# Kernel optimization log

Hardware: AMD Instinct MI355X
Metric: run time of the kernel (lower is better)

Reference implementation:

```python
import jax, jax.numpy as jnp
import numpy as np

B, IN_DIM, UNITS, NUM_K, NUM_S = 4096, 128, 256, 64, 256


def setup_inputs() -> dict:
    key = jax.random.key(0)
    ks = jax.random.split(key, 24)
    d = {
        "X": jax.random.normal(ks[0], (B, IN_DIM), jnp.float32),
        "h_prev": jax.random.normal(ks[1], (B, UNITS), jnp.float32),
        "c_prev": jax.random.normal(ks[2], (B, UNITS), jnp.float32),
        "M_prev": jax.random.normal(ks[3], (B, NUM_K, NUM_S), jnp.float32),
        "k_prev": jax.random.normal(ks[4], (B, NUM_S), jnp.float32),
    }
    rows = IN_DIM + UNITS
    s = 0.05
    d["Wf"] = jax.random.normal(ks[5], (rows, UNITS), jnp.float32) * s
    d["Wt"] = jax.random.normal(ks[6], (rows, UNITS), jnp.float32) * s
    d["Wi"] = jax.random.normal(ks[7], (rows, UNITS), jnp.float32) * s
    d["Wo"] = jax.random.normal(ks[8], (rows, UNITS), jnp.float32) * s
    d["bf"] = jnp.zeros((UNITS,), jnp.float32)
    d["bt"] = jnp.zeros((UNITS,), jnp.float32)
    d["bi"] = jnp.zeros((UNITS,), jnp.float32)
    d["bo"] = jnp.zeros((UNITS,), jnp.float32)
    d["Wk"] = jax.random.normal(ks[9], (UNITS, NUM_S), jnp.float32) * s
    d["bk"] = jnp.zeros((NUM_S,), jnp.float32)
    d["Wr"] = jax.random.normal(ks[10], (NUM_S, UNITS), jnp.float32) * s
    d["Wc"] = jax.random.normal(ks[11], (UNITS, UNITS), jnp.float32) * s
    d["Wh"] = jax.random.normal(ks[12], (NUM_S, UNITS), jnp.float32) * s
    d["We"] = jax.random.normal(ks[13], (UNITS, NUM_S), jnp.float32) * s
    d["be"] = jnp.zeros((NUM_S,), jnp.float32)
    d["Wa"] = jax.random.normal(ks[14], (UNITS, NUM_S), jnp.float32) * s
    d["ba"] = jnp.zeros((NUM_S,), jnp.float32)
    return d


def _l2n(x):
    # matches tf.nn.l2_normalize: x / sqrt(max(sum(x^2), eps))
    return x / jnp.sqrt(jnp.maximum(jnp.sum(x * x, axis=-1, keepdims=True), 1e-12))


def reference(X, h_prev, c_prev, M_prev, k_prev,
              Wf, Wt, Wi, Wo, bf, bt, bi, bo,
              Wk, bk, Wr, Wc, Wh, We, be, Wa, ba):
    sig = jax.nn.sigmoid
    xh = jnp.concatenate([X, h_prev], axis=-1)          # (B, in+units)
    i = sig(xh @ Wi + bi)
    f = sig(xh @ Wf + bf)
    o = sig(xh @ Wo + bo)
    t = sig(xh @ Wt + bt)
    c = f * c_prev + i * t                              # (B, units)

    # tf.keras.losses.cosine_similarity returns NEGATIVE cosine similarity
    cos = jnp.einsum('bks,bs->bk', _l2n(M_prev), _l2n(k_prev))
    alpha = jax.nn.softmax(-cos, axis=-1)               # (B, K)
    r = jnp.einsum('bk,bks->bs', alpha, M_prev)         # content read (B, S)

    rc_1 = sig(r @ Wr + c @ Wc)
    h_curr = o * jnp.tanh(c + rc_1 * (r @ Wh))          # (B, units)

    k_curr = jnp.tanh(h_curr @ Wk + bk)                 # (B, S)
    e = sig(h_curr @ We + be)                           # erase  (B, S)
    a = jnp.tanh(h_curr @ Wa + ba)                      # add    (B, S)
    al = alpha[:, :, None]                              # (B, K, 1)
    M_curr = M_prev * (1.0 - al * e[:, None, :]) + al * a[:, None, :]
    return h_curr, c, M_curr, k_curr
```

## Files before the change

### kernel.cpp

```cpp
#include <hip/hip_runtime.h>
#include <math.h>


#define BATCH 4096
#define INDIM 128
#define UNITS 256
#define NUMK  64
#define NUMS  256

typedef unsigned short u16;
typedef __attribute__((ext_vector_type(4))) float  f32x4;
typedef __attribute__((ext_vector_type(8))) short  s16x8;
typedef __attribute__((ext_vector_type(4))) u16    u16x4;
typedef __attribute__((ext_vector_type(8))) u16    u16x8;

__device__ __forceinline__ float sigf(float x) { return 1.0f / (1.0f + expf(-x)); }

__device__ __forceinline__ u16 f2bf(float x) {
    unsigned u = __float_as_uint(x);
    return (u16)((u + 0x7fffu + ((u >> 16) & 1u)) >> 16);
}
__device__ __forceinline__ float bf2f(u16 h) {
    return __uint_as_float(((unsigned)h) << 16);
}
__device__ __forceinline__ void split_bf(float x, u16& hi, u16& lo) {
    hi = f2bf(x);
    lo = f2bf(x - bf2f(hi));
}

__global__ __launch_bounds__(256) void prep_a1(
    const float* __restrict__ X, const float* __restrict__ hp,
    u16* __restrict__ Ahi, u16* __restrict__ Alo)
{
    const int idx = blockIdx.x * 256 + threadIdx.x;
    const int row = idx / 96;
    const int cg  = (idx - row * 96) * 4;
    float4 v;
    if (cg < INDIM) v = *(const float4*)(X + row * INDIM + cg);
    else            v = *(const float4*)(hp + row * UNITS + (cg - INDIM));
    u16x4 h, l;
    u16 th, tl;
    split_bf(v.x, th, tl); h.x = th; l.x = tl;
    split_bf(v.y, th, tl); h.y = th; l.y = tl;
    split_bf(v.z, th, tl); h.z = th; l.z = tl;
    split_bf(v.w, th, tl); h.w = th; l.w = tl;
    *(u16x4*)(Ahi + row * 384 + cg) = h;
    *(u16x4*)(Alo + row * 384 + cg) = l;
}

__global__ __launch_bounds__(256) void pack_all(
    const float* __restrict__ Wf, const float* __restrict__ Wt,
    const float* __restrict__ Wi, const float* __restrict__ Wo,
    const float* __restrict__ Wr, const float* __restrict__ Wc,
    const float* __restrict__ Wh,
    const float* __restrict__ Wk, const float* __restrict__ We,
    const float* __restrict__ Wa,
    u16* __restrict__ W1hi, u16* __restrict__ W1lo,
    u16* __restrict__ W3hi, u16* __restrict__ W3lo,
    u16* __restrict__ W4hi, u16* __restrict__ W4lo)
{
    const int bid = blockIdx.x;
    if (bid < 192) {
        const int tid = bid * 256 + threadIdx.x;
        const int n  = tid / 48;
        const int k0 = (tid - n * 48) * 8;
        const float* src = (n < 256) ? Wf : (n < 512) ? Wt : (n < 768) ? Wi : Wo;
        const int nc = n & 255;
        u16x8 h, l;
        #pragma unroll
        for (int j = 0; j < 8; ++j) {
            float x = src[(k0 + j) * 256 + nc];
            u16 th, tl;
            split_bf(x, th, tl);
            h[j] = th; l[j] = tl;
        }
        *(u16x8*)(W1hi + n * 384 + k0) = h;
        *(u16x8*)(W1lo + n * 384 + k0) = l;
    } else if (bid < 320) {
        const int tid = (bid - 192) * 256 + threadIdx.x;
        const int n  = tid / 64;
        const int k0 = (tid - n * 64) * 8;
        u16x8 h, l;
        #pragma unroll
        for (int j = 0; j < 8; ++j) {
            const int k = k0 + j;
            float x;
            if (n < 256) x = (k < 256) ? Wr[k * 256 + n] : Wc[(k - 256) * 256 + n];
            else         x = (k < 256) ? Wh[k * 256 + (n - 256)] : 0.0f;
            u16 th, tl;
            split_bf(x, th, tl);
            h[j] = th; l[j] = tl;
        }
        *(u16x8*)(W3hi + n * 512 + k0) = h;
        *(u16x8*)(W3lo + n * 512 + k0) = l;
    } else {
        const int tid = (bid - 320) * 256 + threadIdx.x;
        const int n  = tid / 32;
        const int k0 = (tid - n * 32) * 8;
        const float* src = (n < 256) ? Wk : (n < 512) ? We : Wa;
        const int nc = n & 255;
        u16x8 h, l;
        #pragma unroll
        for (int j = 0; j < 8; ++j) {
            float x = src[(k0 + j) * 256 + nc];
            u16 th, tl;
            split_bf(x, th, tl);
            h[j] = th; l[j] = tl;
        }
        *(u16x8*)(W4hi + n * 256 + k0) = h;
        *(u16x8*)(W4lo + n * 256 + k0) = l;
    }
}

__global__ __launch_bounds__(256) void gemm1_e1(
    const u16* __restrict__ Ahi, const u16* __restrict__ Alo,
    const u16* __restrict__ Bhi, const u16* __restrict__ Blo,
    const float* __restrict__ c_prev,
    const float* __restrict__ bf, const float* __restrict__ bt,
    const float* __restrict__ bi, const float* __restrict__ bo,
    float* __restrict__ c_out, float* __restrict__ o_ws,
    u16* __restrict__ A3hi, u16* __restrict__ A3lo)
{
    const int K = 384;
    const int t = threadIdx.x;
    const int wave = t >> 6, lane = t & 63;
    const int m0 = blockIdx.x * 64 + wave * 16;
    const int col0 = blockIdx.y * 16;
    const int r = lane & 15, g = lane >> 4;

    const u16* pAh = Ahi + (size_t)(m0 + r) * K + g * 8;
    const u16* pAl = Alo + (size_t)(m0 + r) * K + g * 8;
    const u16* pBh = Bhi + (size_t)(col0 + r) * K + g * 8;
    const u16* pBl = Blo + (size_t)(col0 + r) * K + g * 8;

    f32x4 acc[4];
    #pragma unroll
    for (int j = 0; j < 4; ++j) acc[j] = (f32x4){0.f, 0.f, 0.f, 0.f};

    #pragma unroll 2
    for (int k0 = 0; k0 < 384; k0 += 32) {
        s16x8 ah = *(const s16x8*)(pAh + k0);
        s16x8 al = *(const s16x8*)(pAl + k0);
        #pragma unroll
        for (int j = 0; j < 4; ++j) {
            s16x8 bh = *(const s16x8*)(pBh + (size_t)j * 256 * K + k0);
            s16x8 bl = *(const s16x8*)(pBl + (size_t)j * 256 * K + k0);
            acc[j] = __builtin_amdgcn_mfma_f32_16x16x32_bf16(ah, bh, acc[j], 0, 0, 0);
            acc[j] = __builtin_amdgcn_mfma_f32_16x16x32_bf16(al, bh, acc[j], 0, 0, 0);
            acc[j] = __builtin_amdgcn_mfma_f32_16x16x32_bf16(ah, bl, acc[j], 0, 0, 0);
        }
    }

    const int col = col0 + r;
    const float bfv = bf[col], btv = bt[col], biv = bi[col], bov = bo[col];
    #pragma unroll
    for (int rr = 0; rr < 4; ++rr) {
        const int row = m0 + g * 4 + rr;
        const float cp = c_prev[(size_t)row * 256 + col];
        const float f  = sigf(acc[0][rr] + bfv);
        const float tt = sigf(acc[1][rr] + btv);
        const float i  = sigf(acc[2][rr] + biv);
        const float o  = sigf(acc[3][rr] + bov);
        const float cv = f * cp + i * tt;
        c_out[(size_t)row * 256 + col] = cv;
        o_ws [(size_t)row * 256 + col] = o;
        u16 hi, lo;
        split_bf(cv, hi, lo);
        A3hi[(size_t)row * 512 + 256 + col] = hi;
        A3lo[(size_t)row * 512 + 256 + col] = lo;
    }
}

__global__ __launch_bounds__(256) void k2_cosr(
    const float* __restrict__ M, const float* __restrict__ k_prev,
    float* __restrict__ alpha_out, u16* __restrict__ A3hi, u16* __restrict__ A3lo)
{
    const int b = blockIdx.x;
    const int t = threadIdx.x;
    const int lane = t & 63;
    const int w = t >> 6;

    __shared__ float sdot[64][8];
    __shared__ float sssq[64][8];
    __shared__ float salpha[64];
    __shared__ float spr[4][256];

    const float4 k4 = *(const float4*)(k_prev + b * NUMS + lane * 4);
    float kss = k4.x * k4.x + k4.y * k4.y + k4.z * k4.z + k4.w * k4.w;
    #pragma unroll
    for (int m = 1; m < 64; m <<= 1) kss += __shfl_xor(kss, m, 64);
    const float knorm = sqrtf(fmaxf(kss, 1e-12f));

    const float* Mb = M + (size_t)b * (NUMK * NUMS);
    f32x4 mreg[16];
    #pragma unroll
    for (int j = 0; j < 16; ++j)
        mreg[j] = *(const f32x4*)(Mb + (w * 16 + j) * NUMS + lane * 4);

    #pragma unroll
    for (int j = 0; j < 16; ++j) {
        const f32x4 m4 = mreg[j];
        float dot = m4.x * k4.x + m4.y * k4.y + m4.z * k4.z + m4.w * k4.w;
        float ssq = m4.x * m4.x + m4.y * m4.y + m4.z * m4.z + m4.w * m4.w;
        #pragma unroll
        for (int m = 1; m < 8; m <<= 1) {
            dot += __shfl_xor(dot, m, 64);
            ssq += __shfl_xor(ssq, m, 64);
        }
        if ((lane & 7) == 0) {
            sdot[w * 16 + j][lane >> 3] = dot;
            sssq[w * 16 + j][lane >> 3] = ssq;
        }
    }
    __syncthreads();

    if (t < 64) {
        float dot = 0.f, ssq = 0.f;
        #pragma unroll
        for (int q = 0; q < 8; ++q) { dot += sdot[t][q]; ssq += sssq[t][q]; }
        const float cosv = dot / (sqrtf(fmaxf(ssq, 1e-12f)) * knorm);
        float v = -cosv;
        float vmax = v;
        #pragma unroll
        for (int m = 1; m < 64; m <<= 1) vmax = fmaxf(vmax, __shfl_xor(vmax, m, 64));
        float e = expf(v - vmax);
        float s = e;
        #pragma unroll
        for (int m = 1; m < 64; m <<= 1) s += __shfl_xor(s, m, 64);
        const float al = e / s;
        salpha[t] = al;
        alpha_out[b * NUMK + t] = al;
    }
    __syncthreads();

    float pr0 = 0.f, pr1 = 0.f, pr2 = 0.f, pr3 = 0.f;
    #pragma unroll
    for (int j = 0; j < 16; ++j) {
        const float al = salpha[w * 16 + j];
        pr0 = fmaf(al, mreg[j].x, pr0);
        pr1 = fmaf(al, mreg[j].y, pr1);
        pr2 = fmaf(al, mreg[j].z, pr2);
        pr3 = fmaf(al, mreg[j].w, pr3);
    }
    *(float4*)&spr[w][lane * 4] = make_float4(pr0, pr1, pr2, pr3);
    __syncthreads();
    const float rv = spr[0][t] + spr[1][t] + spr[2][t] + spr[3][t];
    u16 hi, lo;
    split_bf(rv, hi, lo);
    A3hi[(size_t)b * 512 + t] = hi;
    A3lo[(size_t)b * 512 + t] = lo;
}

__global__ __launch_bounds__(256) void gemm3_e2(
    const u16* __restrict__ Ahi, const u16* __restrict__ Alo,
    const u16* __restrict__ Bhi, const u16* __restrict__ Blo,
    const float* __restrict__ c, const float* __restrict__ o,
    float* __restrict__ h_out, u16* __restrict__ A4hi, u16* __restrict__ A4lo)
{
    const int K = 512;
    const int t = threadIdx.x;
    const int wave = t >> 6, lane = t & 63;
    const int m0 = blockIdx.x * 64 + wave * 16;
    const int col0 = blockIdx.y * 16;
    const int r = lane & 15, g = lane >> 4;

    const u16* pAh = Ahi + (size_t)(m0 + r) * K + g * 8;
    const u16* pAl = Alo + (size_t)(m0 + r) * K + g * 8;
    const u16* pBh = Bhi + (size_t)(col0 + r) * K + g * 8;
    const u16* pBl = Blo + (size_t)(col0 + r) * K + g * 8;

    f32x4 acc[2];
    acc[0] = (f32x4){0.f, 0.f, 0.f, 0.f};
    acc[1] = (f32x4){0.f, 0.f, 0.f, 0.f};

    #pragma unroll 2
    for (int k0 = 0; k0 < 512; k0 += 32) {
        s16x8 ah = *(const s16x8*)(pAh + k0);
        s16x8 al = *(const s16x8*)(pAl + k0);
        #pragma unroll
        for (int j = 0; j < 2; ++j) {
            s16x8 bh = *(const s16x8*)(pBh + (size_t)j * 256 * K + k0);
            s16x8 bl = *(const s16x8*)(pBl + (size_t)j * 256 * K + k0);
            acc[j] = __builtin_amdgcn_mfma_f32_16x16x32_bf16(ah, bh, acc[j], 0, 0, 0);
            acc[j] = __builtin_amdgcn_mfma_f32_16x16x32_bf16(al, bh, acc[j], 0, 0, 0);
            acc[j] = __builtin_amdgcn_mfma_f32_16x16x32_bf16(ah, bl, acc[j], 0, 0, 0);
        }
    }

    const int col = col0 + r;
    #pragma unroll
    for (int rr = 0; rr < 4; ++rr) {
        const int row = m0 + g * 4 + rr;
        const float cv = c[(size_t)row * 256 + col];
        const float ov = o[(size_t)row * 256 + col];
        const float hv = ov * tanhf(cv + sigf(acc[0][rr]) * acc[1][rr]);
        h_out[(size_t)row * 256 + col] = hv;
        u16 hi, lo;
        split_bf(hv, hi, lo);
        A4hi[(size_t)row * 256 + col] = hi;
        A4lo[(size_t)row * 256 + col] = lo;
    }
}

__global__ __launch_bounds__(256) void gemm4_e3(
    const u16* __restrict__ Ahi, const u16* __restrict__ Alo,
    const u16* __restrict__ Bhi, const u16* __restrict__ Blo,
    const float* __restrict__ bk, const float* __restrict__ be,
    const float* __restrict__ ba,
    float* __restrict__ k_out, float* __restrict__ e_ws, float* __restrict__ a_ws)
{
    const int K = 256;
    const int t = threadIdx.x;
    const int wave = t >> 6, lane = t & 63;
    const int m0 = blockIdx.x * 64 + wave * 16;
    const int col0 = blockIdx.y * 16;
    const int r = lane & 15, g = lane >> 4;

    const u16* pAh = Ahi + (size_t)(m0 + r) * K + g * 8;
    const u16* pAl = Alo + (size_t)(m0 + r) * K + g * 8;
    const u16* pBh = Bhi + (size_t)(col0 + r) * K + g * 8;
    const u16* pBl = Blo + (size_t)(col0 + r) * K + g * 8;

    f32x4 acc[3];
    #pragma unroll
    for (int j = 0; j < 3; ++j) acc[j] = (f32x4){0.f, 0.f, 0.f, 0.f};

    #pragma unroll 2
    for (int k0 = 0; k0 < 256; k0 += 32) {
        s16x8 ah = *(const s16x8*)(pAh + k0);
        s16x8 al = *(const s16x8*)(pAl + k0);
        #pragma unroll
        for (int j = 0; j < 3; ++j) {
            s16x8 bh = *(const s16x8*)(pBh + (size_t)j * 256 * K + k0);
            s16x8 bl = *(const s16x8*)(pBl + (size_t)j * 256 * K + k0);
            acc[j] = __builtin_amdgcn_mfma_f32_16x16x32_bf16(ah, bh, acc[j], 0, 0, 0);
            acc[j] = __builtin_amdgcn_mfma_f32_16x16x32_bf16(al, bh, acc[j], 0, 0, 0);
            acc[j] = __builtin_amdgcn_mfma_f32_16x16x32_bf16(ah, bl, acc[j], 0, 0, 0);
        }
    }

    const int col = col0 + r;
    const float bkv = bk[col], bev = be[col], bav = ba[col];
    #pragma unroll
    for (int rr = 0; rr < 4; ++rr) {
        const int row = m0 + g * 4 + rr;
        k_out[(size_t)row * 256 + col] = tanhf(acc[0][rr] + bkv);
        e_ws [(size_t)row * 256 + col] = sigf (acc[1][rr] + bev);
        a_ws [(size_t)row * 256 + col] = tanhf(acc[2][rr] + bav);
    }
}

__global__ __launch_bounds__(256) void k5_mup(
    const float* __restrict__ M, const float* __restrict__ alpha,
    const float* __restrict__ e, const float* __restrict__ a,
    float* __restrict__ Mout)
{
    const int b = blockIdx.x;
    const int t = threadIdx.x;
    __shared__ float sal[64];
    if (t < 64) sal[t] = alpha[b * NUMK + t];

    const int s4 = (t & 63) * 4;
    const int kr = t >> 6;
    const float4 e4 = *(const float4*)(e + b * NUMS + s4);
    const float4 a4 = *(const float4*)(a + b * NUMS + s4);
    __syncthreads();

    const float* Mb = M + (size_t)b * (NUMK * NUMS);
    float* Ob = Mout + (size_t)b * (NUMK * NUMS);
    #pragma unroll
    for (int j = 0; j < 16; ++j) {
        const int k = j * 4 + kr;
        const float al = sal[k];
        f32x4 m4 = *(const f32x4*)(Mb + k * NUMS + s4);
        f32x4 o4;
        o4.x = m4.x * (1.0f - al * e4.x) + al * a4.x;
        o4.y = m4.y * (1.0f - al * e4.y) + al * a4.y;
        o4.z = m4.z * (1.0f - al * e4.z) + al * a4.z;
        o4.w = m4.w * (1.0f - al * e4.w) + al * a4.w;
        __builtin_nontemporal_store(o4, (f32x4*)(Ob + k * NUMS + s4));
    }
}

extern "C" void kernel_launch(void* const* d_in, const int* in_sizes, int n_in,
                              void* d_out, int out_size, void* d_ws, size_t ws_size,
                              hipStream_t stream)
{
    (void)in_sizes; (void)n_in; (void)out_size; (void)ws_size;

    const float* X      = (const float*)d_in[0];
    const float* h_prev = (const float*)d_in[1];
    const float* c_prev = (const float*)d_in[2];
    const float* M_prev = (const float*)d_in[3];
    const float* k_prev = (const float*)d_in[4];
    const float* Wf = (const float*)d_in[5];
    const float* Wt = (const float*)d_in[6];
    const float* Wi = (const float*)d_in[7];
    const float* Wo = (const float*)d_in[8];
    const float* bf = (const float*)d_in[9];
    const float* bt = (const float*)d_in[10];
    const float* bi = (const float*)d_in[11];
    const float* bo = (const float*)d_in[12];
    const float* Wk = (const float*)d_in[13];
    const float* bk = (const float*)d_in[14];
    const float* Wr = (const float*)d_in[15];
    const float* Wc = (const float*)d_in[16];
    const float* Wh = (const float*)d_in[17];
    const float* We = (const float*)d_in[18];
    const float* be = (const float*)d_in[19];
    const float* Wa = (const float*)d_in[20];
    const float* ba = (const float*)d_in[21];

    float* out = (float*)d_out;
    float* h_out = out;
    float* c_out = out + 1048576;
    float* M_out = out + 2097152;
    float* k_out = out + 69206016;

    char* w = (char*)d_ws;
    size_t off = 0;
    auto carve = [&](size_t bytes) { void* p = w + off; off += (bytes + 255) & ~(size_t)255; return p; };
    u16* A1hi = (u16*)carve(4096ull * 384 * 2);
    u16* A1lo = (u16*)carve(4096ull * 384 * 2);
    u16* W1hi = (u16*)carve(1024ull * 384 * 2);
    u16* W1lo = (u16*)carve(1024ull * 384 * 2);
    u16* W3hi = (u16*)carve(512ull * 512 * 2);
    u16* W3lo = (u16*)carve(512ull * 512 * 2);
    u16* W4hi = (u16*)carve(768ull * 256 * 2);
    u16* W4lo = (u16*)carve(768ull * 256 * 2);
    u16* A3hi = (u16*)carve(4096ull * 512 * 2);
    u16* A3lo = (u16*)carve(4096ull * 512 * 2);
    u16* A4hi = (u16*)carve(4096ull * 256 * 2);
    u16* A4lo = (u16*)carve(4096ull * 256 * 2);
    float* o_ws  = (float*)carve(4096ull * 256 * 4);
    float* al_ws = (float*)carve(4096ull * 64 * 4);
    float* e_ws  = (float*)carve(4096ull * 256 * 4);
    float* a_ws  = (float*)carve(4096ull * 256 * 4);

    pack_all<<<416, 256, 0, stream>>>(Wf, Wt, Wi, Wo, Wr, Wc, Wh, Wk, We, Wa,
                                      W1hi, W1lo, W3hi, W3lo, W4hi, W4lo);
    prep_a1<<<1536, 256, 0, stream>>>(X, h_prev, A1hi, A1lo);

    gemm1_e1<<<dim3(64, 16), 256, 0, stream>>>(A1hi, A1lo, W1hi, W1lo, c_prev,
                                               bf, bt, bi, bo,
                                               c_out, o_ws, A3hi, A3lo);

    k2_cosr<<<4096, 256, 0, stream>>>(M_prev, k_prev, al_ws, A3hi, A3lo);

    gemm3_e2<<<dim3(64, 16), 256, 0, stream>>>(A3hi, A3lo, W3hi, W3lo,
                                               c_out, o_ws, h_out, A4hi, A4lo);

    gemm4_e3<<<dim3(64, 16), 256, 0, stream>>>(A4hi, A4lo, W4hi, W4lo,
                                               bk, be, ba, k_out, e_ws, a_ws);

    k5_mup<<<4096, 256, 0, stream>>>(M_prev, al_ws, e_ws, a_ws, M_out);
}
```

Before: 697.3 us.

## Merge prep kernels and co-schedule cosine-read with first GEMM in one launch

Combines the weight-packing and activation-splitting kernels into a single launch, and fuses the memory-read (cosine/softmax/read) kernel with the gate GEMM into one grid so the two independent stages run concurrently. It also reverses the batch order in the memory-update kernel, presumably so the rows most recently read (and likely still in cache) are processed first. This cuts launch count and lets the bandwidth-bound and MFMA-bound work overlap, at the cost of a larger shared-memory footprint applied to the GEMM blocks too.

```diff
diff --git a/kernel.cpp b/kernel.cpp
--- a/kernel.cpp
+++ b/kernel.cpp
@@ -28,40 +28,37 @@
     lo = f2bf(x - bf2f(hi));
 }
 
-__global__ __launch_bounds__(256) void prep_a1(
+__global__ __launch_bounds__(256) void prep_all(
     const float* __restrict__ X, const float* __restrict__ hp,
-    u16* __restrict__ Ahi, u16* __restrict__ Alo)
-{
-    const int idx = blockIdx.x * 256 + threadIdx.x;
-    const int row = idx / 96;
-    const int cg  = (idx - row * 96) * 4;
-    float4 v;
-    if (cg < INDIM) v = *(const float4*)(X + row * INDIM + cg);
-    else            v = *(const float4*)(hp + row * UNITS + (cg - INDIM));
-    u16x4 h, l;
-    u16 th, tl;
-    split_bf(v.x, th, tl); h.x = th; l.x = tl;
-    split_bf(v.y, th, tl); h.y = th; l.y = tl;
-    split_bf(v.z, th, tl); h.z = th; l.z = tl;
-    split_bf(v.w, th, tl); h.w = th; l.w = tl;
-    *(u16x4*)(Ahi + row * 384 + cg) = h;
-    *(u16x4*)(Alo + row * 384 + cg) = l;
-}
-
-__global__ __launch_bounds__(256) void pack_all(
     const float* __restrict__ Wf, const float* __restrict__ Wt,
     const float* __restrict__ Wi, const float* __restrict__ Wo,
     const float* __restrict__ Wr, const float* __restrict__ Wc,
     const float* __restrict__ Wh,
     const float* __restrict__ Wk, const float* __restrict__ We,
     const float* __restrict__ Wa,
+    u16* __restrict__ A1hi, u16* __restrict__ A1lo,
     u16* __restrict__ W1hi, u16* __restrict__ W1lo,
     u16* __restrict__ W3hi, u16* __restrict__ W3lo,
     u16* __restrict__ W4hi, u16* __restrict__ W4lo)
 {
     const int bid = blockIdx.x;
-    if (bid < 192) {
-        const int tid = bid * 256 + threadIdx.x;
+    if (bid < 1536) {
+        const int idx = bid * 256 + threadIdx.x;
+        const int row = idx / 96;
+        const int cg  = (idx - row * 96) * 4;
+        float4 v;
+        if (cg < INDIM) v = *(const float4*)(X + row * INDIM + cg);
+        else            v = *(const float4*)(hp + row * UNITS + (cg - INDIM));
+        u16x4 h, l;
+        u16 th, tl;
+        split_bf(v.x, th, tl); h.x = th; l.x = tl;
+        split_bf(v.y, th, tl); h.y = th; l.y = tl;
+        split_bf(v.z, th, tl); h.z = th; l.z = tl;
+        split_bf(v.w, th, tl); h.w = th; l.w = tl;
+        *(u16x4*)(A1hi + row * 384 + cg) = h;
+        *(u16x4*)(A1lo + row * 384 + cg) = l;
+    } else if (bid < 1728) {
+        const int tid = (bid - 1536) * 256 + threadIdx.x;
         const int n  = tid / 48;
         const int k0 = (tid - n * 48) * 8;
         const float* src = (n < 256) ? Wf : (n < 512) ? Wt : (n < 768) ? Wi : Wo;
@@ -76,8 +73,8 @@
         }
         *(u16x8*)(W1hi + n * 384 + k0) = h;
         *(u16x8*)(W1lo + n * 384 + k0) = l;
-    } else if (bid < 320) {
-        const int tid = (bid - 192) * 256 + threadIdx.x;
+    } else if (bid < 1856) {
+        const int tid = (bid - 1728) * 256 + threadIdx.x;
         const int n  = tid / 64;
         const int k0 = (tid - n * 64) * 8;
         u16x8 h, l;
@@ -94,7 +91,7 @@
         *(u16x8*)(W3hi + n * 512 + k0) = h;
         *(u16x8*)(W3lo + n * 512 + k0) = l;
     } else {
-        const int tid = (bid - 320) * 256 + threadIdx.x;
+        const int tid = (bid - 1856) * 256 + threadIdx.x;
         const int n  = tid / 32;
         const int k0 = (tid - n * 32) * 8;
         const float* src = (n < 256) ? Wk : (n < 512) ? We : Wa;
@@ -112,7 +109,9 @@
     }
 }
 
-__global__ __launch_bounds__(256) void gemm1_e1(
+__global__ __launch_bounds__(256) void mega1(
+    const float* __restrict__ M, const float* __restrict__ k_prev,
+    float* __restrict__ alpha_out,
     const u16* __restrict__ Ahi, const u16* __restrict__ Alo,
     const u16* __restrict__ Bhi, const u16* __restrict__ Blo,
     const float* __restrict__ c_prev,
@@ -121,134 +120,131 @@
     float* __restrict__ c_out, float* __restrict__ o_ws,
     u16* __restrict__ A3hi, u16* __restrict__ A3lo)
 {
-    const int K = 384;
     const int t = threadIdx.x;
-    const int wave = t >> 6, lane = t & 63;
-    const int m0 = blockIdx.x * 64 + wave * 16;
-    const int col0 = blockIdx.y * 16;
-    const int r = lane & 15, g = lane >> 4;
-
-    const u16* pAh = Ahi + (size_t)(m0 + r) * K + g * 8;
-    const u16* pAl = Alo + (size_t)(m0 + r) * K + g * 8;
-    const u16* pBh = Bhi + (size_t)(col0 + r) * K + g * 8;
-    const u16* pBl = Blo + (size_t)(col0 + r) * K + g * 8;
-
-    f32x4 acc[4];
-    #pragma unroll
-    for (int j = 0; j < 4; ++j) acc[j] = (f32x4){0.f, 0.f, 0.f, 0.f};
-
-    #pragma unroll 2
-    for (int k0 = 0; k0 < 384; k0 += 32) {
-        s16x8 ah = *(const s16x8*)(pAh + k0);
-        s16x8 al = *(const s16x8*)(pAl + k0);
-        #pragma unroll
-        for (int j = 0; j < 4; ++j) {
-            s16x8 bh = *(const s16x8*)(pBh + (size_t)j * 256 * K + k0);
-            s16x8 bl = *(const s16x8*)(pBl + (size_t)j * 256 * K + k0);
-            acc[j] = __builtin_amdgcn_mfma_f32_16x16x32_bf16(ah, bh, acc[j], 0, 0, 0);
-            acc[j] = __builtin_amdgcn_mfma_f32_16x16x32_bf16(al, bh, acc[j], 0, 0, 0);
-            acc[j] = __builtin_amdgcn_mfma_f32_16x16x32_bf16(ah, bl, acc[j], 0, 0, 0);
-        }
-    }
-
-    const int col = col0 + r;
-    const float bfv = bf[col], btv = bt[col], biv = bi[col], bov = bo[col];
-    #pragma unroll
-    for (int rr = 0; rr < 4; ++rr) {
-        const int row = m0 + g * 4 + rr;
-        const float cp = c_prev[(size_t)row * 256 + col];
-        const float f  = sigf(acc[0][rr] + bfv);
-        const float tt = sigf(acc[1][rr] + btv);
-        const float i  = sigf(acc[2][rr] + biv);
-        const float o  = sigf(acc[3][rr] + bov);
-        const float cv = f * cp + i * tt;
-        c_out[(size_t)row * 256 + col] = cv;
-        o_ws [(size_t)row * 256 + col] = o;
+    if (blockIdx.x < 4096) {
+        const int b = blockIdx.x;
+        const int lane = t & 63;
+        const int w = t >> 6;
+
+        __shared__ float sdot[64][8];
+        __shared__ float sssq[64][8];
+        __shared__ float salpha[64];
+        __shared__ float spr[4][256];
+
+        const float4 k4 = *(const float4*)(k_prev + b * NUMS + lane * 4);
+        float kss = k4.x * k4.x + k4.y * k4.y + k4.z * k4.z + k4.w * k4.w;
+        #pragma unroll
+        for (int m = 1; m < 64; m <<= 1) kss += __shfl_xor(kss, m, 64);
+        const float knorm = sqrtf(fmaxf(kss, 1e-12f));
+
+        const float* Mb = M + (size_t)b * (NUMK * NUMS);
+        f32x4 mreg[16];
+        #pragma unroll
+        for (int j = 0; j < 16; ++j)
+            mreg[j] = *(const f32x4*)(Mb + (w * 16 + j) * NUMS + lane * 4);
+
+        #pragma unroll
+        for (int j = 0; j < 16; ++j) {
+            const f32x4 m4 = mreg[j];
+            float dot = m4.x * k4.x + m4.y * k4.y + m4.z * k4.z + m4.w * k4.w;
+            float ssq = m4.x * m4.x + m4.y * m4.y + m4.z * m4.z + m4.w * m4.w;
+            #pragma unroll
+            for (int m = 1; m < 8; m <<= 1) {
+                dot += __shfl_xor(dot, m, 64);
+                ssq += __shfl_xor(ssq, m, 64);
+            }
+            if ((lane & 7) == 0) {
+                sdot[w * 16 + j][lane >> 3] = dot;
+                sssq[w * 16 + j][lane >> 3] = ssq;
+            }
+        }
+        __syncthreads();
+
+        if (t < 64) {
+            float dot = 0.f, ssq = 0.f;
+            #pragma unroll
+            for (int q = 0; q < 8; ++q) { dot += sdot[t][q]; ssq += sssq[t][q]; }
+            const float cosv = dot / (sqrtf(fmaxf(ssq, 1e-12f)) * knorm);
+            float v = -cosv;
+            float vmax = v;
+            #pragma unroll
+            for (int m = 1; m < 64; m <<= 1) vmax = fmaxf(vmax, __shfl_xor(vmax, m, 64));
+            float e = expf(v - vmax);
+            float s = e;
+            #pragma unroll
+            for (int m = 1; m < 64; m <<= 1) s += __shfl_xor(s, m, 64);
+            const float al = e / s;
+            salpha[t] = al;
+            alpha_out[b * NUMK + t] = al;
+        }
+        __syncthreads();
+
+        float pr0 = 0.f, pr1 = 0.f, pr2 = 0.f, pr3 = 0.f;
+        #pragma unroll
+        for (int j = 0; j < 16; ++j) {
+            const float al = salpha[w * 16 + j];
+            pr0 = fmaf(al, mreg[j].x, pr0);
+            pr1 = fmaf(al, mreg[j].y, pr1);
+            pr2 = fmaf(al, mreg[j].z, pr2);
+            pr3 = fmaf(al, mreg[j].w, pr3);
+        }
+        *(float4*)&spr[w][lane * 4] = make_float4(pr0, pr1, pr2, pr3);
+        __syncthreads();
+        const float rv = spr[0][t] + spr[1][t] + spr[2][t] + spr[3][t];
         u16 hi, lo;
-        split_bf(cv, hi, lo);
-        A3hi[(size_t)row * 512 + 256 + col] = hi;
-        A3lo[(size_t)row * 512 + 256 + col] = lo;
-    }
-}
-
-__global__ __launch_bounds__(256) void k2_cosr(
-    const float* __restrict__ M, const float* __restrict__ k_prev,
-    float* __restrict__ alpha_out, u16* __restrict__ A3hi, u16* __restrict__ A3lo)
-{
-    const int b = blockIdx.x;
-    const int t = threadIdx.x;
-    const int lane = t & 63;
-    const int w = t >> 6;
-
-    __shared__ float sdot[64][8];
-    __shared__ float sssq[64][8];
-    __shared__ float salpha[64];
-    __shared__ float spr[4][256];
-
-    const float4 k4 = *(const float4*)(k_prev + b * NUMS + lane * 4);
-    float kss = k4.x * k4.x + k4.y * k4.y + k4.z * k4.z + k4.w * k4.w;
-    #pragma unroll
-    for (int m = 1; m < 64; m <<= 1) kss += __shfl_xor(kss, m, 64);
-    const float knorm = sqrtf(fmaxf(kss, 1e-12f));
-
-    const float* Mb = M + (size_t)b * (NUMK * NUMS);
-    f32x4 mreg[16];
-    #pragma unroll
-    for (int j = 0; j < 16; ++j)
-        mreg[j] = *(const f32x4*)(Mb + (w * 16 + j) * NUMS + lane * 4);
-
-    #pragma unroll
-    for (int j = 0; j < 16; ++j) {
-        const f32x4 m4 = mreg[j];
-        float dot = m4.x * k4.x + m4.y * k4.y + m4.z * k4.z + m4.w * k4.w;
-        float ssq = m4.x * m4.x + m4.y * m4.y + m4.z * m4.z + m4.w * m4.w;
-        #pragma unroll
-        for (int m = 1; m < 8; m <<= 1) {
-            dot += __shfl_xor(dot, m, 64);
-            ssq += __shfl_xor(ssq, m, 64);
-        }
-        if ((lane & 7) == 0) {
-            sdot[w * 16 + j][lane >> 3] = dot;
-            sssq[w * 16 + j][lane >> 3] = ssq;
-        }
-    }
-    __syncthreads();
-
-    if (t < 64) {
-        float dot = 0.f, ssq = 0.f;
-        #pragma unroll
-        for (int q = 0; q < 8; ++q) { dot += sdot[t][q]; ssq += sssq[t][q]; }
-        const float cosv = dot / (sqrtf(fmaxf(ssq, 1e-12f)) * knorm);
-        float v = -cosv;
-        float vmax = v;
-        #pragma unroll
-        for (int m = 1; m < 64; m <<= 1) vmax = fmaxf(vmax, __shfl_xor(vmax, m, 64));
-        float e = expf(v - vmax);
-        float s = e;
-        #pragma unroll
-        for (int m = 1; m < 64; m <<= 1) s += __shfl_xor(s, m, 64);
-        const float al = e / s;
-        salpha[t] = al;
-        alpha_out[b * NUMK + t] = al;
-    }
-    __syncthreads();
-
-    float pr0 = 0.f, pr1 = 0.f, pr2 = 0.f, pr3 = 0.f;
-    #pragma unroll
-    for (int j = 0; j < 16; ++j) {
-        const float al = salpha[w * 16 + j];
-        pr0 = fmaf(al, mreg[j].x, pr0);
-        pr1 = fmaf(al, mreg[j].y, pr1);
-        pr2 = fmaf(al, mreg[j].z, pr2);
-        pr3 = fmaf(al, mreg[j].w, pr3);
-    }
-    *(float4*)&spr[w][lane * 4] = make_float4(pr0, pr1, pr2, pr3);
-    __syncthreads();
-    const float rv = spr[0][t] + spr[1][t] + spr[2][t] + spr[3][t];
-    u16 hi, lo;
-    split_bf(rv, hi, lo);
-    A3hi[(size_t)b * 512 + t] = hi;
-    A3lo[(size_t)b * 512 + t] = lo;
+        split_bf(rv, hi, lo);
+        A3hi[(size_t)b * 512 + t] = hi;
+        A3lo[(size_t)b * 512 + t] = lo;
+    } else {
+        const int K = 384;
+        const int bid = blockIdx.x - 4096;
+        const int wave = t >> 6, lane = t & 63;
+        const int m0 = (bid >> 4) * 64 + wave * 16;
+        const int col0 = (bid & 15) * 16;
+        const int r = lane & 15, g = lane >> 4;
+
+        const u16* pAh = Ahi + (size_t)(m0 + r) * K + g * 8;
+        const u16* pAl = Alo + (size_t)(m0 + r) * K + g * 8;
+        const u16* pBh = Bhi + (size_t)(col0 + r) * K + g * 8;
+        const u16* pBl = Blo + (size_t)(col0 + r) * K + g * 8;
+
+        f32x4 acc[4];
+        #pragma unroll
+        for (int j = 0; j < 4; ++j) acc[j] = (f32x4){0.f, 0.f, 0.f, 0.f};
+
+        #pragma unroll 2
+        for (int k0 = 0; k0 < 384; k0 += 32) {
+            s16x8 ah = *(const s16x8*)(pAh + k0);
+            s16x8 al = *(const s16x8*)(pAl + k0);
+            #pragma unroll
+            for (int j = 0; j < 4; ++j) {
+                s16x8 bh = *(const s16x8*)(pBh + (size_t)j * 256 * K + k0);
+                s16x8 bl = *(const s16x8*)(pBl + (size_t)j * 256 * K + k0);
+                acc[j] = __builtin_amdgcn_mfma_f32_16x16x32_bf16(ah, bh, acc[j], 0, 0, 0);
+                acc[j] = __builtin_amdgcn_mfma_f32_16x16x32_bf16(al, bh, acc[j], 0, 0, 0);
+                acc[j] = __builtin_amdgcn_mfma_f32_16x16x32_bf16(ah, bl, acc[j], 0, 0, 0);
+            }
+        }
+
+        const int col = col0 + r;
+        const float bfv = bf[col], btv = bt[col], biv = bi[col], bov = bo[col];
+        #pragma unroll
+        for (int rr = 0; rr < 4; ++rr) {
+            const int row = m0 + g * 4 + rr;
+            const float cp = c_prev[(size_t)row * 256 + col];
+            const float f  = sigf(acc[0][rr] + bfv);
+            const float tt = sigf(acc[1][rr] + btv);
+            const float i  = sigf(acc[2][rr] + biv);
+            const float o  = sigf(acc[3][rr] + bov);
+            const float cv = f * cp + i * tt;
+            c_out[(size_t)row * 256 + col] = cv;
+            o_ws [(size_t)row * 256 + col] = o;
+            u16 hi, lo;
+            split_bf(cv, hi, lo);
+            A3hi[(size_t)row * 512 + 256 + col] = hi;
+            A3lo[(size_t)row * 512 + 256 + col] = lo;
+        }
+    }
 }
 
 __global__ __launch_bounds__(256) void gemm3_e2(
@@ -355,7 +351,7 @@
     const float* __restrict__ e, const float* __restrict__ a,
     float* __restrict__ Mout)
 {
-    const int b = blockIdx.x;
+    const int b = 4095 - blockIdx.x;
     const int t = threadIdx.x;
     __shared__ float sal[64];
     if (t < 64) sal[t] = alpha[b * NUMK + t];
@@ -437,15 +433,14 @@
     float* e_ws  = (float*)carve(4096ull * 256 * 4);
     float* a_ws  = (float*)carve(4096ull * 256 * 4);
 
-    pack_all<<<416, 256, 0, stream>>>(Wf, Wt, Wi, Wo, Wr, Wc, Wh, Wk, We, Wa,
-                                      W1hi, W1lo, W3hi, W3lo, W4hi, W4lo);
-    prep_a1<<<1536, 256, 0, stream>>>(X, h_prev, A1hi, A1lo);
-
-    gemm1_e1<<<dim3(64, 16), 256, 0, stream>>>(A1hi, A1lo, W1hi, W1lo, c_prev,
-                                               bf, bt, bi, bo,
-                                               c_out, o_ws, A3hi, A3lo);
-
-    k2_cosr<<<4096, 256, 0, stream>>>(M_prev, k_prev, al_ws, A3hi, A3lo);
+    prep_all<<<1952, 256, 0, stream>>>(X, h_prev, Wf, Wt, Wi, Wo, Wr, Wc, Wh,
+                                       Wk, We, Wa,
+                                       A1hi, A1lo, W1hi, W1lo, W3hi, W3lo, W4hi, W4lo);
+
+    mega1<<<5120, 256, 0, stream>>>(M_prev, k_prev, al_ws,
+                                    A1hi, A1lo, W1hi, W1lo, c_prev,
+                                    bf, bt, bi, bo,
+                                    c_out, o_ws, A3hi, A3lo);
 
     gemm3_e2<<<dim3(64, 16), 256, 0, stream>>>(A3hi, A3lo, W3hi, W3lo,
                                                c_out, o_ws, h_out, A4hi, A4lo);
```

Result: faster. 681.9 us (-2.2%).
